# Performance work log

Hardware: AMD Instinct MI355X
Metric: run time of the kernel (lower is better)

The kernel has to match this reference:

```python
import jax, jax.numpy as jnp
import numpy as np

R = 0.25
M = 0


def setup_inputs() -> dict:
    key = jax.random.key(0)
    k1, k2, k3, k4 = jax.random.split(key, 4)
    B, T_cmp, C = 2, 4096, 4096
    H, KVH, D, W = 32, 8, 128, 512
    return {
        "x_m": jax.random.normal(k1, (B, 2 * T_cmp, C), dtype=jnp.float32),
        "xm_cmp": jax.random.normal(k2, (B, T_cmp, C), dtype=jnp.float32),
        "q_w": jax.random.normal(k3, (B, H, W, D), dtype=jnp.float32),
        "km_cmp": jax.random.normal(k4, (B, KVH, T_cmp, D), dtype=jnp.float32),
    }


def reference(x_m, xm_cmp, q_w, km_cmp):
    B, T_cmp, C = xm_cmp.shape
    groups = q_w.shape[1] // km_cmp.shape[1]  # GQA repeat factor
    scaling = q_w.shape[-1] ** -0.5

    # importance_score: repeat kv heads, scaled-dot attention, softmax over keys,
    # sum over query positions, mean over heads -> [B, T_cmp]
    km = jnp.repeat(km_cmp, groups, axis=1)  # [B, H, T_cmp, D]
    scores = jnp.einsum('bhqd,bhkd->bhqk', q_w, km) * scaling
    weights = jax.nn.softmax(scores, axis=-1)
    importance = weights.sum(axis=2).mean(axis=1)  # [B, T_cmp]

    # select_indices: static top-k count
    k = min(int(R * T_cmp + M * (1 - R) / 2), T_cmp)
    _, idx = jax.lax.top_k(importance, k)  # [B, k]

    # interleave_selected: selected compressed tokens are replaced by their
    # two original tokens x_m[2t], x_m[2t+1]; others keep xm_cmp[t].
    b_idx = jnp.arange(B)[:, None]
    expand_mask = jnp.zeros((B, T_cmp), dtype=bool).at[b_idx, idx].set(True)
    sizes = jnp.where(expand_mask, 2, 1)
    start = jnp.cumsum(sizes, axis=1) - sizes  # output start position per token
    T_out = T_cmp + k

    first = jnp.where(expand_mask[..., None], x_m[:, ::2], xm_cmp)  # [B,T_cmp,C]
    second = x_m[:, 1::2]  # [B, T_cmp, C]
    pos2 = jnp.where(expand_mask, start + 1, T_out)  # non-expanded -> dummy slot

    y = jnp.zeros((B, T_out + 1, C), dtype=xm_cmp.dtype)
    y = y.at[b_idx, start].set(first)
    y = y.at[b_idx, pos2].set(second)
    return y[:, :T_out]
```

## Files before the change

kernel.cpp:

```cpp
#include <hip/hip_runtime.h>
#include <hip/hip_bf16.h>

#define B_    2
#define H_    32
#define KVH_  8
#define T_    4096
#define C_    4096
#define D_    128
#define W_    512
#define KTOP  1024
#define TOUT  (T_ + KTOP)
#define QB    64
#define NQB   (W_/QB)
#define TB    64
#define NTT   (T_/TB)
#define NPART (H_*NQB)
#define NBLK  (NQB*H_*B_)
#define SCALE 0.08838834764831845f

typedef __attribute__((ext_vector_type(8))) _Float16 half8;
typedef __attribute__((ext_vector_type(4))) float f32x4;

__device__ __forceinline__ void gload16(const void* g, void* l) {
    __builtin_amdgcn_global_load_lds(
        (const __attribute__((address_space(1))) void*)g,
        (__attribute__((address_space(3))) void*)l, 16, 0, 0);
}

__global__ __launch_bounds__(256) void convert_k_kernel(
    const float* __restrict__ km, _Float16* __restrict__ Khw,
    _Float16* __restrict__ Klw)
{
    int g = blockIdx.x*256 + threadIdx.x;
    size_t e = (size_t)g*8;
    int d0 = (int)(e & 127);
    size_t row = e >> 7;
    int t = (int)(row & (T_-1));
    size_t bk = row >> 12;
    int r = t & 63, tt = t >> 6;
    size_t off = (bk<<19) + (size_t)tt*(TB*D_) + (size_t)r*D_ + (d0 ^ ((r&7)<<3));
    float4 v0 = *(const float4*)(km + e);
    float4 v1 = *(const float4*)(km + e + 4);
    float f[8] = {v0.x,v0.y,v0.z,v0.w,v1.x,v1.y,v1.z,v1.w};
    half8 hh, hl;
#pragma unroll
    for (int i = 0; i < 8; ++i) {
        _Float16 hi = (_Float16)f[i];
        hh[i] = hi;
        hl[i] = (_Float16)(f[i] - (float)hi);
    }
    *(half8*)&Khw[off] = hh;
    *(half8*)&Klw[off] = hl;
}

#define STAGE(bufidx, tt)                                                   \
    {                                                                       \
        gload16(gh0 + (size_t)(tt)*8192,        &sKh[bufidx][ldsoff]);      \
        gload16(gh0 + (size_t)(tt)*8192 + 4096, &sKh[bufidx][4096+ldsoff]); \
        gload16(gl0 + (size_t)(tt)*8192,        &sKl[bufidx][ldsoff]);      \
        gload16(gl0 + (size_t)(tt)*8192 + 4096, &sKl[bufidx][4096+ldsoff]); \
    }

#define PIPE_HEAD(NTILES)                                                   \
    if (tt + 1 < (NTILES)) {                                                \
        STAGE(cur^1, tt+1);                                                 \
        asm volatile("s_waitcnt vmcnt(4)" ::: "memory");                    \
    } else {                                                                \
        asm volatile("s_waitcnt vmcnt(0)" ::: "memory");                    \
    }                                                                       \
    __builtin_amdgcn_s_barrier();

#define PIPE_TAIL()                                                         \
    asm volatile("" ::: "memory");                                          \
    __builtin_amdgcn_s_barrier();                                           \
    cur ^= 1;

#define TILE_MFMA(bufidx, acc)                                              \
    {                                                                       \
        const _Float16* bKh = sKh[bufidx];                                  \
        const _Float16* bKl = sKl[bufidx];                                  \
        const int rr = kg*16 + li;                                          \
        const int rx = (rr & 7) << 3;                                       \
        _Pragma("unroll")                                                   \
        for (int ks2 = 0; ks2 < 4; ++ks2) {                                 \
            const int off = rr*D_ + ((ks2*32 + lg*8) ^ rx);                 \
            half8 bh = *(const half8*)&bKh[off];                            \
            half8 bl = *(const half8*)&bKl[off];                            \
            _Pragma("unroll")                                               \
            for (int mm = 0; mm < 2; ++mm) {                                \
                acc[mm] = __builtin_amdgcn_mfma_f32_16x16x32_f16(qh[mm][ks2], bh, acc[mm], 0,0,0); \
                acc[mm] = __builtin_amdgcn_mfma_f32_16x16x32_f16(ql[mm][ks2], bh, acc[mm], 0,0,0); \
                acc[mm] = __builtin_amdgcn_mfma_f32_16x16x32_f16(qh[mm][ks2], bl, acc[mm], 0,0,0); \
            }                                                               \
        }                                                                   \
    }

__global__ __launch_bounds__(512, 2) void fused_imp_kernel(
    const float* __restrict__ q_w, const _Float16* __restrict__ Khw,
    const _Float16* __restrict__ Klw, float* __restrict__ partial)
{
    __shared__ __align__(16) _Float16 sKh[2][TB*D_];
    __shared__ __align__(16) _Float16 sKl[2][TB*D_];
    __shared__ float sL[2][4][32];
    __shared__ float sR[2][32];
    __shared__ float sTmp[2][2][64];

    const int tid = threadIdx.x, wid = tid >> 6, lane = tid & 63;
    const int lg = lane >> 4, li = lane & 15;
    const int qg = wid >> 2, kg = wid & 3;

    const int flat = blockIdx.x;
    const int xcd = flat & 7, m = flat >> 3;
    const int g = (m >> 5)*8 + xcd;
    const int r = m & 31;
    const int kvh = g & 7, b = g >> 3;
    const int hh = r >> 3, qb = r & 7;
    const int h = kvh*4 + hh;

    half8 qh[2][4], ql[2][4];
    {
        const float* qp0 = q_w + (((size_t)b*H_ + h)*W_ + qb*QB + qg*32 + li)*D_;
#pragma unroll
        for (int mm = 0; mm < 2; ++mm)
#pragma unroll
            for (int ks2 = 0; ks2 < 4; ++ks2) {
                const float* p = qp0 + mm*16*D_ + ks2*32 + lg*8;
                float4 v0 = *(const float4*)p;
                float4 v1 = *(const float4*)(p+4);
                float f[8] = {v0.x,v0.y,v0.z,v0.w,v1.x,v1.y,v1.z,v1.w};
#pragma unroll
                for (int e = 0; e < 8; ++e) {
                    _Float16 hv = (_Float16)f[e];
                    qh[mm][ks2][e] = hv;
                    ql[mm][ks2][e] = (_Float16)(f[e] - (float)hv);
                }
            }
    }

    const size_t kvoff = ((size_t)b*KVH_ + kvh) * ((size_t)T_*D_);
    const _Float16* gh0 = Khw + kvoff + (size_t)tid*8;
    const _Float16* gl0 = Klw + kvoff + (size_t)tid*8;
    const int ldsoff = wid*512 + lane*8;

    float lacc[2][4] = {};
    STAGE(0, 0);
    int cur = 0;
    for (int tt = 0; tt < NTT; ++tt) {
        PIPE_HEAD(NTT);
        f32x4 acc[2];
#pragma unroll
        for (int mm = 0; mm < 2; ++mm) acc[mm] = (f32x4){0.f,0.f,0.f,0.f};
        TILE_MFMA(cur, acc);
#pragma unroll
        for (int mm = 0; mm < 2; ++mm)
#pragma unroll
            for (int j = 0; j < 4; ++j)
                lacc[mm][j] += __expf(acc[mm][j]*SCALE);
        PIPE_TAIL();
    }
#pragma unroll
    for (int mm = 0; mm < 2; ++mm)
#pragma unroll
        for (int j = 0; j < 4; ++j) {
            float v = lacc[mm][j];
            v += __shfl_xor(v, 1); v += __shfl_xor(v, 2);
            v += __shfl_xor(v, 4); v += __shfl_xor(v, 8);
            if (li == 0) sL[qg][kg][mm*16 + lg*4 + j] = v;
        }
    __syncthreads();
    if (tid < 64) {
        int qg2 = tid >> 5, ql2 = tid & 31;
        float l = sL[qg2][0][ql2] + sL[qg2][1][ql2]
                + sL[qg2][2][ql2] + sL[qg2][3][ql2];
        sR[qg2][ql2] = 1.0f / l;
    }
    __syncthreads();
    float rv[2][4];
#pragma unroll
    for (int mm = 0; mm < 2; ++mm)
#pragma unroll
        for (int j = 0; j < 4; ++j)
            rv[mm][j] = sR[qg][mm*16 + lg*4 + j];

    const size_t po = (((size_t)(h*NQB + qb))*B_ + b)*T_;
    STAGE(0, 0);
    cur = 0;
    for (int tt = 0; tt < NTT; ++tt) {
        PIPE_HEAD(NTT);
        f32x4 acc[2];
#pragma unroll
        for (int mm = 0; mm < 2; ++mm) acc[mm] = (f32x4){0.f,0.f,0.f,0.f};
        TILE_MFMA(cur, acc);
        float x = 0.f;
#pragma unroll
        for (int mm = 0; mm < 2; ++mm)
#pragma unroll
            for (int j = 0; j < 4; ++j)
                x += __expf(acc[mm][j]*SCALE)*rv[mm][j];
        x += __shfl_xor(x, 16); x += __shfl_xor(x, 32);
        if (lg == 0) sTmp[tt & 1][qg][kg*16 + li] = x;
        if (tt > 0 && tid < 64) {
            float s = sTmp[(tt-1)&1][0][tid] + sTmp[(tt-1)&1][1][tid];
            partial[po + (size_t)(tt-1)*TB + tid] = s;
        }
        PIPE_TAIL();
    }
    if (tid < 64) {
        float s = sTmp[(NTT-1)&1][0][tid] + sTmp[(NTT-1)&1][1][tid];
        partial[po + (size_t)(NTT-1)*TB + tid] = s;
    }
}

__global__ __launch_bounds__(256) void imp_reduce_kernel(
    const float* __restrict__ partial, float* __restrict__ imp)
{
    int gid = blockIdx.x*256 + threadIdx.x;
    int b = gid >> 12, t = gid & (T_-1);
    float s = 0.f;
    for (int i = 0; i < NPART; ++i)
        s += partial[((size_t)(i*B_ + b))*T_ + t];
    imp[gid] = s * (1.0f/H_);
}

__global__ __launch_bounds__(1024) void topk_kernel(
    const float* __restrict__ imp, int* __restrict__ mask, int* __restrict__ start)
{
    __shared__ int hist[256];
    __shared__ int sa[1024], sb[1024];
    __shared__ int sbin, srem;
    const int tid = threadIdx.x, b = blockIdx.x;
    const int i0 = 4*tid;

    unsigned key[4];
#pragma unroll
    for (int j = 0; j < 4; ++j) {
        unsigned u = __float_as_uint(imp[b*T_ + i0 + j]);
        key[j] = (u & 0x80000000u) ? ~u : (u | 0x80000000u);
    }

    unsigned prefix = 0;
    int k_rem = KTOP;
#pragma unroll
    for (int sh = 24; sh >= 0; sh -= 8) {
        unsigned hi_mask = (sh == 24) ? 0u : (0xFFFFFFFFu << (sh + 8));
        if (tid < 256) hist[tid] = 0;
        __syncthreads();
#pragma unroll
        for (int j = 0; j < 4; ++j)
            if ((key[j] & hi_mask) == prefix)
                atomicAdd(&hist[(key[j] >> sh) & 255], 1);
        __syncthreads();
        if (tid == 0) {
            int acc = 0, bin = 255;
            for (; bin > 0; --bin) {
                int hv = hist[bin];
                if (acc + hv >= k_rem) break;
                acc += hv;
            }
            sbin = bin; srem = k_rem - acc;
        }
        __syncthreads();
        prefix |= ((unsigned)sbin) << sh;
        k_rem = srem;
        __syncthreads();
    }

    int m[4], eq[4];
#pragma unroll
    for (int j = 0; j < 4; ++j) {
        m[j]  = key[j] > prefix ? 1 : 0;
        eq[j] = (key[j] == prefix) ? 1 : 0;
    }
    int e4 = eq[0]+eq[1]+eq[2]+eq[3];
    sa[tid] = e4;
    __syncthreads();
    {
        int *src = sa, *dst = sb;
        for (int off = 1; off < 1024; off <<= 1) {
            int v = src[tid];
            if (tid >= off) v += src[tid - off];
            dst[tid] = v;
            __syncthreads();
            int* t2 = src; src = dst; dst = t2;
        }
        int r = src[tid] - e4;
#pragma unroll
        for (int j = 0; j < 4; ++j) {
            if (eq[j] && r < k_rem) m[j] = 1;
            r += eq[j];
        }
    }
    __syncthreads();
    int s4 = m[0]+m[1]+m[2]+m[3];
    sa[tid] = s4;
    __syncthreads();
    int *src = sa, *dst = sb;
    for (int off = 1; off < 1024; off <<= 1) {
        int v = src[tid];
        if (tid >= off) v += src[tid - off];
        dst[tid] = v;
        __syncthreads();
        int* t2 = src; src = dst; dst = t2;
    }
    int excl = src[tid] - s4;
    start[b*T_+i0+0] = i0+0 + excl;
    start[b*T_+i0+1] = i0+1 + excl + m[0];
    start[b*T_+i0+2] = i0+2 + excl + m[0]+m[1];
    start[b*T_+i0+3] = i0+3 + excl + m[0]+m[1]+m[2];
    mask[b*T_+i0+0] = m[0]; mask[b*T_+i0+1] = m[1];
    mask[b*T_+i0+2] = m[2]; mask[b*T_+i0+3] = m[3];
}

__global__ __launch_bounds__(256) void scatter_kernel(
    const float* __restrict__ x_m, const float* __restrict__ xm_cmp,
    const int* __restrict__ mask, const int* __restrict__ start,
    float* __restrict__ out)
{
    const int t = blockIdx.x, b = blockIdx.y, tid = threadIdx.x;
    const int mk = mask[b*T_+t];
    const int st = start[b*T_+t];
    const float* s1 = mk ? (x_m + ((size_t)b*2*T_ + 2*t)*C_)
                         : (xm_cmp + ((size_t)b*T_ + t)*C_);
    float4* d1 = (float4*)(out + ((size_t)b*TOUT + st)*C_);
    const float4* s1v = (const float4*)s1;
    for (int i = tid; i < C_/4; i += 256) d1[i] = s1v[i];
    if (mk) {
        const float4* s2v = (const float4*)(x_m + ((size_t)b*2*T_ + 2*t+1)*C_);
        float4* d2 = d1 + C_/4;
        for (int i = tid; i < C_/4; i += 256) d2[i] = s2v[i];
    }
}

extern "C" void kernel_launch(void* const* d_in, const int* in_sizes, int n_in,
                              void* d_out, int out_size, void* d_ws, size_t ws_size,
                              hipStream_t stream)
{
    (void)in_sizes; (void)n_in; (void)out_size; (void)ws_size;
    const float* x_m    = (const float*)d_in[0];
    const float* xm_cmp = (const float*)d_in[1];
    const float* q_w    = (const float*)d_in[2];
    const float* km     = (const float*)d_in[3];
    float* out = (float*)d_out;

    char* ws = (char*)d_ws;
    _Float16* Khw   = (_Float16*)ws;
    _Float16* Klw   = (_Float16*)(ws + 16777216);
    float* partial  = (float*)(ws + 33554432);
    float* imp      = (float*)(ws + 41943040);
    int*   mask     = (int*)  (ws + 41975808);
    int*   start    = (int*)  (ws + 42008576);

    convert_k_kernel<<<dim3(4096), dim3(256), 0, stream>>>(km, Khw, Klw);
    fused_imp_kernel<<<dim3(NBLK), dim3(512), 0, stream>>>(q_w, Khw, Klw, partial);
    imp_reduce_kernel<<<dim3((B_*T_)/256), dim3(256), 0, stream>>>(partial, imp);
    topk_kernel<<<dim3(B_), dim3(1024), 0, stream>>>(imp, mask, start);
    scatter_kernel<<<dim3(T_, B_), dim3(256), 0, stream>>>(x_m, xm_cmp, mask, start, out);
}
```

Before: 323.0 us.

## Use 4 waves per block, each covering all 64 queries per key subtile

The fused importance kernel drops from 8 waves in a 2x4 query/key split to 4 waves. Each wave now holds all 64 query rows (4 MFMA row groups) against its 16-key slice. Every B-operand LDS read is reused across twice as many MFMAs, and the cross-query-group LDS combine before writing partial sums is gone, so each wave writes its slice straight to global. The cost is doubled per-wave register use for Q fragments and accumulators, which risks lower occupancy, and each thread now issues twice as many async loads per tile.

Result: faster. 314.7 us (-2.5%).

```diff
diff --git a/kernel.cpp b/kernel.cpp
--- a/kernel.cpp
+++ b/kernel.cpp
@@ -55,16 +55,22 @@
 
 #define STAGE(bufidx, tt)                                                   \
     {                                                                       \
-        gload16(gh0 + (size_t)(tt)*8192,        &sKh[bufidx][ldsoff]);      \
-        gload16(gh0 + (size_t)(tt)*8192 + 4096, &sKh[bufidx][4096+ldsoff]); \
-        gload16(gl0 + (size_t)(tt)*8192,        &sKl[bufidx][ldsoff]);      \
-        gload16(gl0 + (size_t)(tt)*8192 + 4096, &sKl[bufidx][4096+ldsoff]); \
+        const _Float16* gh_ = gh0 + (size_t)(tt)*8192;                      \
+        const _Float16* gl_ = gl0 + (size_t)(tt)*8192;                      \
+        gload16(gh_,        &sKh[bufidx][ldsoff]);                          \
+        gload16(gh_ + 2048, &sKh[bufidx][ldsoff + 2048]);                   \
+        gload16(gh_ + 4096, &sKh[bufidx][ldsoff + 4096]);                   \
+        gload16(gh_ + 6144, &sKh[bufidx][ldsoff + 6144]);                   \
+        gload16(gl_,        &sKl[bufidx][ldsoff]);                          \
+        gload16(gl_ + 2048, &sKl[bufidx][ldsoff + 2048]);                   \
+        gload16(gl_ + 4096, &sKl[bufidx][ldsoff + 4096]);                   \
+        gload16(gl_ + 6144, &sKl[bufidx][ldsoff + 6144]);                   \
     }
 
 #define PIPE_HEAD(NTILES)                                                   \
     if (tt + 1 < (NTILES)) {                                                \
         STAGE(cur^1, tt+1);                                                 \
-        asm volatile("s_waitcnt vmcnt(4)" ::: "memory");                    \
+        asm volatile("s_waitcnt vmcnt(8)" ::: "memory");                    \
     } else {                                                                \
         asm volatile("s_waitcnt vmcnt(0)" ::: "memory");                    \
     }                                                                       \
@@ -87,7 +93,7 @@
             half8 bh = *(const half8*)&bKh[off];                            \
             half8 bl = *(const half8*)&bKl[off];                            \
             _Pragma("unroll")                                               \
-            for (int mm = 0; mm < 2; ++mm) {                                \
+            for (int mm = 0; mm < 4; ++mm) {                                \
                 acc[mm] = __builtin_amdgcn_mfma_f32_16x16x32_f16(qh[mm][ks2], bh, acc[mm], 0,0,0); \
                 acc[mm] = __builtin_amdgcn_mfma_f32_16x16x32_f16(ql[mm][ks2], bh, acc[mm], 0,0,0); \
                 acc[mm] = __builtin_amdgcn_mfma_f32_16x16x32_f16(qh[mm][ks2], bl, acc[mm], 0,0,0); \
@@ -95,19 +101,18 @@
         }                                                                   \
     }
 
-__global__ __launch_bounds__(512, 2) void fused_imp_kernel(
+__global__ __launch_bounds__(256, 2) void fused_imp_kernel(
     const float* __restrict__ q_w, const _Float16* __restrict__ Khw,
     const _Float16* __restrict__ Klw, float* __restrict__ partial)
 {
     __shared__ __align__(16) _Float16 sKh[2][TB*D_];
     __shared__ __align__(16) _Float16 sKl[2][TB*D_];
-    __shared__ float sL[2][4][32];
-    __shared__ float sR[2][32];
-    __shared__ float sTmp[2][2][64];
+    __shared__ float sL[4][QB];
+    __shared__ float sR[QB];
 
     const int tid = threadIdx.x, wid = tid >> 6, lane = tid & 63;
     const int lg = lane >> 4, li = lane & 15;
-    const int qg = wid >> 2, kg = wid & 3;
+    const int kg = wid;
 
     const int flat = blockIdx.x;
     const int xcd = flat & 7, m = flat >> 3;
@@ -117,11 +122,11 @@
     const int hh = r >> 3, qb = r & 7;
     const int h = kvh*4 + hh;
 
-    half8 qh[2][4], ql[2][4];
+    half8 qh[4][4], ql[4][4];
     {
-        const float* qp0 = q_w + (((size_t)b*H_ + h)*W_ + qb*QB + qg*32 + li)*D_;
-#pragma unroll
-        for (int mm = 0; mm < 2; ++mm)
+        const float* qp0 = q_w + (((size_t)b*H_ + h)*W_ + qb*QB + li)*D_;
+#pragma unroll
+        for (int mm = 0; mm < 4; ++mm)
 #pragma unroll
             for (int ks2 = 0; ks2 < 4; ++ks2) {
                 const float* p = qp0 + mm*16*D_ + ks2*32 + lg*8;
@@ -140,74 +145,65 @@
     const size_t kvoff = ((size_t)b*KVH_ + kvh) * ((size_t)T_*D_);
     const _Float16* gh0 = Khw + kvoff + (size_t)tid*8;
     const _Float16* gl0 = Klw + kvoff + (size_t)tid*8;
-    const int ldsoff = wid*512 + lane*8;
-
-    float lacc[2][4] = {};
+    const int ldsoff = tid*8;
+
+    float lacc[4][4] = {};
     STAGE(0, 0);
     int cur = 0;
     for (int tt = 0; tt < NTT; ++tt) {
         PIPE_HEAD(NTT);
-        f32x4 acc[2];
-#pragma unroll
-        for (int mm = 0; mm < 2; ++mm) acc[mm] = (f32x4){0.f,0.f,0.f,0.f};
+        f32x4 acc[4];
+#pragma unroll
+        for (int mm = 0; mm < 4; ++mm) acc[mm] = (f32x4){0.f,0.f,0.f,0.f};
         TILE_MFMA(cur, acc);
 #pragma unroll
-        for (int mm = 0; mm < 2; ++mm)
+        for (int mm = 0; mm < 4; ++mm)
 #pragma unroll
             for (int j = 0; j < 4; ++j)
                 lacc[mm][j] += __expf(acc[mm][j]*SCALE);
         PIPE_TAIL();
     }
 #pragma unroll
-    for (int mm = 0; mm < 2; ++mm)
+    for (int mm = 0; mm < 4; ++mm)
 #pragma unroll
         for (int j = 0; j < 4; ++j) {
             float v = lacc[mm][j];
             v += __shfl_xor(v, 1); v += __shfl_xor(v, 2);
             v += __shfl_xor(v, 4); v += __shfl_xor(v, 8);
-            if (li == 0) sL[qg][kg][mm*16 + lg*4 + j] = v;
+            if (li == 0) sL[kg][mm*16 + lg*4 + j] = v;
         }
     __syncthreads();
-    if (tid < 64) {
-        int qg2 = tid >> 5, ql2 = tid & 31;
-        float l = sL[qg2][0][ql2] + sL[qg2][1][ql2]
-                + sL[qg2][2][ql2] + sL[qg2][3][ql2];
-        sR[qg2][ql2] = 1.0f / l;
-    }
-    __syncthreads();
-    float rv[2][4];
-#pragma unroll
-    for (int mm = 0; mm < 2; ++mm)
+    if (tid < QB) {
+        float l = sL[0][tid] + sL[1][tid] + sL[2][tid] + sL[3][tid];
+        sR[tid] = 1.0f / l;
+    }
+    __syncthreads();
+    float rv[4][4];
+#pragma unroll
+    for (int mm = 0; mm < 4; ++mm)
 #pragma unroll
         for (int j = 0; j < 4; ++j)
-            rv[mm][j] = sR[qg][mm*16 + lg*4 + j];
+            rv[mm][j] = sR[mm*16 + lg*4 + j];
 
     const size_t po = (((size_t)(h*NQB + qb))*B_ + b)*T_;
     STAGE(0, 0);
     cur = 0;
     for (int tt = 0; tt < NTT; ++tt) {
         PIPE_HEAD(NTT);
-        f32x4 acc[2];
-#pragma unroll
-        for (int mm = 0; mm < 2; ++mm) acc[mm] = (f32x4){0.f,0.f,0.f,0.f};
+        f32x4 acc[4];
+#pragma unroll
+        for (int mm = 0; mm < 4; ++mm) acc[mm] = (f32x4){0.f,0.f,0.f,0.f};
         TILE_MFMA(cur, acc);
         float x = 0.f;
 #pragma unroll
-        for (int mm = 0; mm < 2; ++mm)
+        for (int mm = 0; mm < 4; ++mm)
 #pragma unroll
             for (int j = 0; j < 4; ++j)
                 x += __expf(acc[mm][j]*SCALE)*rv[mm][j];
         x += __shfl_xor(x, 16); x += __shfl_xor(x, 32);
-        if (lg == 0) sTmp[tt & 1][qg][kg*16 + li] = x;
-        if (tt > 0 && tid < 64) {
-            float s = sTmp[(tt-1)&1][0][tid] + sTmp[(tt-1)&1][1][tid];
-            partial[po + (size_t)(tt-1)*TB + tid] = s;
-        }
+        if (lg == 0)
+            partial[po + (size_t)tt*TB + kg*16 + li] = x;
         PIPE_TAIL();
-    }
-    if (tid < 64) {
-        float s = sTmp[(NTT-1)&1][0][tid] + sTmp[(NTT-1)&1][1][tid];
-        partial[po + (size_t)(NTT-1)*TB + tid] = s;
     }
 }
 
@@ -351,7 +347,7 @@
     int*   start    = (int*)  (ws + 42008576);
 
     convert_k_kernel<<<dim3(4096), dim3(256), 0, stream>>>(km, Khw, Klw);
-    fused_imp_kernel<<<dim3(NBLK), dim3(512), 0, stream>>>(q_w, Khw, Klw, partial);
+    fused_imp_kernel<<<dim3(NBLK), dim3(256), 0, stream>>>(q_w, Khw, Klw, partial);
     imp_reduce_kernel<<<dim3((B_*T_)/256), dim3(256), 0, stream>>>(partial, imp);
     topk_kernel<<<dim3(B_), dim3(1024), 0, stream>>>(imp, mask, start);
     scatter_kernel<<<dim3(T_, B_), dim3(256), 0, stream>>>(x_m, xm_cmp, mask, start, out);
```
